# Kernel tuning notes

Measured on AMD Instinct MI355X. Metric: run time of the kernel, lower is better.

## Reference

```python
import jax, jax.numpy as jnp
import numpy as np

HEADS = 16
EPS = 1e-5

def _ln(t):
    # LayerNorm over last axis, no affine params
    mu = jnp.mean(t, axis=-1, keepdims=True)
    var = jnp.var(t, axis=-1, keepdims=True)
    return (t - mu) / jnp.sqrt(var + EPS)

def setup_inputs() -> dict:
    key = jax.random.key(0)
    ks = jax.random.split(key, 8)
    b, n, dim, mlp_dim = 4, 2048, 1024, 4096
    s = lambda d: 1.0 / np.sqrt(d)
    return {
        "x": jax.random.normal(ks[0], (b, n, dim), dtype=jnp.float32),
        "Wqkv": jax.random.uniform(ks[1], (dim, 3 * dim), jnp.float32, -s(dim), s(dim)),
        "W1": jax.random.uniform(ks[2], (dim, mlp_dim), jnp.float32, -s(dim), s(dim)),
        "b1": jax.random.uniform(ks[3], (mlp_dim,), jnp.float32, -s(dim), s(dim)),
        "W2": jax.random.uniform(ks[4], (mlp_dim, dim), jnp.float32, -s(mlp_dim), s(mlp_dim)),
        "b2": jax.random.uniform(ks[5], (dim,), jnp.float32, -s(mlp_dim), s(mlp_dim)),
        "Wout": jax.random.uniform(ks[6], (dim, dim), jnp.float32, -s(dim), s(dim)),
        "bout": jax.random.uniform(ks[7], (dim,), jnp.float32, -s(dim), s(dim)),
    }

def reference(x, Wqkv, W1, b1, W2, b2, Wout, bout):
    b, n, dim = x.shape
    h = HEADS
    d = dim // h
    scale = dim ** (-0.5)  # NOTE: module scales by full dim, not head_dim
    qkv = x @ Wqkv  # [b, n, 3*dim]
    qkv = qkv.reshape(b, n, 3, h, d).transpose(2, 0, 3, 1, 4)  # [3, b, h, n, d]
    q, k, v = qkv[0], qkv[1], qkv[2]
    q, k = _ln(q), _ln(k)
    dots = jnp.einsum('bhid,bhjd->bhij', q, k) * scale
    attn = jax.nn.softmax(dots, axis=-1)
    attn_v = jnp.einsum('bhij,bhjd->bhid', attn, v)
    attn_v = attn_v.transpose(0, 2, 1, 3).reshape(b, n, dim)
    attn_out = attn_v @ Wout + bout
    parallel = jax.nn.gelu(x @ W1 + b1, approximate=False) @ W2 + b2
    return _ln(attn_out + parallel)
```

## Files before the change

### kernel.cpp

```cpp
#include <hip/hip_runtime.h>

typedef __attribute__((ext_vector_type(8))) short s16x8;
typedef __attribute__((ext_vector_type(4))) short s16x4;
typedef __attribute__((ext_vector_type(4))) float f32x4;
typedef __attribute__((ext_vector_type(16))) float f32x16;
typedef __attribute__((ext_vector_type(2))) unsigned uint2v;

#define DEVINL __device__ __forceinline__

DEVINL float b2f(short u){ return __uint_as_float(((unsigned)(unsigned short)u) << 16); }
DEVINL short f2bf(float f){
  unsigned u = __float_as_uint(f);
  u += 0x7fffu + ((u >> 16) & 1u);
  return (short)(u >> 16);
}
DEVINL unsigned cvtpk(float lo, float hi){
  unsigned r;
  asm("v_cvt_pk_bf16_f32 %0, %1, %2" : "=v"(r) : "v"(lo), "v"(hi));
  return r;
}
DEVINL float max3f(float a, float b, float c){
  float r; asm("v_max3_f32 %0, %1, %2, %3" : "=v"(r) : "v"(a), "v"(b), "v"(c)); return r;
}

#if __has_builtin(__builtin_amdgcn_exp2f)
#define EXP2F __builtin_amdgcn_exp2f
#else
#define EXP2F exp2f
#endif

DEVINL f32x4 mfma32(s16x8 a, s16x8 b, f32x4 c){
  return __builtin_amdgcn_mfma_f32_16x16x32_bf16(a, b, c, 0, 0, 0);
}
DEVINL f32x16 mfma3216(s16x8 a, s16x8 b, f32x16 c){
  return __builtin_amdgcn_mfma_f32_32x32x16_bf16(a, b, c, 0, 0, 0);
}

DEVINL uint2v pl32swap(unsigned a, unsigned b){
#if __has_builtin(__builtin_amdgcn_permlane32_swap)
  return __builtin_amdgcn_permlane32_swap(a, b, false, false);
#else
  asm volatile("v_permlane32_swap_b32 %0, %1" : "+v"(a), "+v"(b));
  uint2v r; r[0] = a; r[1] = b; return r;
#endif
}

typedef const unsigned __attribute__((address_space(1)))* gas1;
typedef unsigned __attribute__((address_space(3)))* las3;
DEVINL void gload16(const short* g, short* l){
  __builtin_amdgcn_global_load_lds((gas1)g, (las3)l, 16, 0, 0);
}

#define CFENCE asm volatile("" ::: "memory")
#define PBAR  do{ CFENCE; __builtin_amdgcn_sched_barrier(0); __builtin_amdgcn_s_barrier(); \
                  __builtin_amdgcn_sched_barrier(0); CFENCE; }while(0)
#define VMW8 asm volatile("s_waitcnt vmcnt(8)" ::: "memory")
#define VMW4 asm volatile("s_waitcnt vmcnt(4)" ::: "memory")
#define VMW0 asm volatile("s_waitcnt vmcnt(0)" ::: "memory")
#define PRIO1 __builtin_amdgcn_s_setprio(1)
#define PRIO0 __builtin_amdgcn_s_setprio(0)

static const int Bc   = 4;
static const int Nc   = 2048;
static const int DIM  = 1024;
static const int Tc   = Bc * Nc;
static const int MLP  = 4096;
static const int D3   = 3072;

static const size_t OFF_XB    = 0;
static const size_t OFF_W1T   = 16777216;
static const size_t OFF_QLN   = 25165824;
static const size_t OFF_KLN   = 41943040;
static const size_t OFF_VT    = 58720256;
static const size_t OFF_ATTNV = 75497472;
static const size_t OFF_HB    = 92274688;
static const size_t OFF_WQKVT = OFF_HB;
static const size_t OFF_W2T   = 0;
static const size_t OFF_WOUTT = 8388608;
static const size_t OFF_S2    = OFF_QLN;

DEVINL void transp_body(const float* __restrict__ W, short* __restrict__ Wt,
                        int K, int N, int bid){
  __shared__ float tile[32][33];
  int ntx = N >> 5;
  int tx = bid % ntx, ty = bid / ntx;
  int r = threadIdx.x >> 3, c = (threadIdx.x & 7) * 4;
  f32x4 v = *(const f32x4*)(W + (size_t)(ty*32 + r)*N + tx*32 + c);
  tile[r][c] = v[0]; tile[r][c+1] = v[1]; tile[r][c+2] = v[2]; tile[r][c+3] = v[3];
  __syncthreads();
  s16x4 o;
#pragma unroll
  for (int j = 0; j < 4; ++j) o[j] = f2bf(tile[c+j][r]);
  *(s16x4*)(Wt + (size_t)(tx*32 + r)*K + ty*32 + c) = o;
}

__global__ __launch_bounds__(256) void prep1(const float* __restrict__ x, short* __restrict__ xb,
                                             const float* __restrict__ Wqkv, short* __restrict__ wqkvt,
                                             const float* __restrict__ W1, short* __restrict__ w1t){
  const int b = blockIdx.x;
  if (b < 4096){
    size_t i = ((size_t)b * 256 + threadIdx.x) * 8;
    f32x4 v0 = *(const f32x4*)(x + i);
    f32x4 v1 = *(const f32x4*)(x + i + 4);
    s16x8 o;
#pragma unroll
    for (int j = 0; j < 4; ++j){ o[j] = f2bf(v0[j]); o[4+j] = f2bf(v1[j]); }
    *(s16x8*)(xb + i) = o;
  } else if (b < 7168){
    transp_body(Wqkv, wqkvt, DIM, D3, b - 4096);
  } else {
    transp_body(W1, w1t, DIM, MLP, b - 7168);
  }
}

__global__ __launch_bounds__(256) void prep2(const float* __restrict__ W2, short* __restrict__ w2t,
                                             const float* __restrict__ Wout, short* __restrict__ woutt){
  const int b = blockIdx.x;
  if (b < 4096) transp_body(W2, w2t, MLP, DIM, b);
  else          transp_body(Wout, woutt, DIM, DIM, b - 4096);
}

template<int ACT, int FUSED, int QKVEPI>
__global__ __launch_bounds__(256, 2) void gemmCF(const short* __restrict__ A, const short* __restrict__ A2,
                                                 const short* __restrict__ Bt, const short* __restrict__ Bt2,
                                                 short* __restrict__ C,
                                                 const float* __restrict__ bias, const float* __restrict__ bias2,
                                                 int M, int N, int K1, int K2,
                                                 short* __restrict__ qln, short* __restrict__ kln,
                                                 short* __restrict__ vtb){
  __shared__ short lds[32768];

  const int tid = threadIdx.x;
  const int w = tid >> 6, lane = tid & 63;
  const int lr = lane & 15, g = lane >> 4;
  const int wr = w >> 1, wc = w & 1;
  const int NT1 = K1 >> 6;
  const int NT = NT1 + (FUSED ? (K2 >> 6) : 0);
  const int NIT = NT >> 1;

  const int nbn = N >> 7;
  const int cpx = gridDim.x >> 3;
  const int bid = (int)blockIdx.x;
  const int sw = (bid & 7)*cpx + (bid >> 3);
  const int nbn8 = nbn >> 3;
  const int T8 = sw >> 6, t64 = sw & 63;
  const int bm = (T8 / nbn8)*8 + (t64 >> 3);
  const int bn = (T8 % nbn8)*8 + (t64 & 7);

  const int l2 = lane >> 2;
  const int gsw = ((lane & 3) - ((lane >> 3) & 3)) & 3;
  const int cof = gsw * 8;
  const int qsw8 = ((g + (lr >> 1)) & 3) * 8;

  const short* ap0h = A  + (size_t)(bm*128 + w*16 + l2)*K1 + cof;
  const short* bp0h = Bt + (size_t)(bn*128 + w*16 + l2)*K1 + cof;
  const short* ap0a = FUSED ? (A2  + (size_t)(bm*128 + w*16 + l2)*K2 + cof) : nullptr;
  const short* bp0a = FUSED ? (Bt2 + (size_t)(bn*128 + w*16 + l2)*K2 + cof) : nullptr;

  auto stA = [&](int s, int T_, int kk){
    short* d0 = lds + s*4096 + w*512;
    if (FUSED && T_ >= NT1){
      size_t off = (size_t)(T_ - NT1)*64 + kk*32;
      gload16(ap0a + off, d0);
      gload16(ap0a + (size_t)64*K2 + off, d0 + 2048);
    } else {
      size_t off = (size_t)T_*64 + kk*32;
      gload16(ap0h + off, d0);
      gload16(ap0h + (size_t)64*K1 + off, d0 + 2048);
    }
  };
  auto stB = [&](int s, int T_, int kk){
    short* d0 = lds + 16384 + s*4096 + w*512;
    if (FUSED && T_ >= NT1){
      size_t off = (size_t)(T_ - NT1)*64 + kk*32;
      gload16(bp0a + off, d0);
      gload16(bp0a + (size_t)64*K2 + off, d0 + 2048);
    } else {
      size_t off = (size_t)T_*64 + kk*32;
      gload16(bp0h + off, d0);
      gload16(bp0h + (size_t)64*K1 + off, d0 + 2048);
    }
  };

#define LDA(s, mi) (*(const s16x8*)&lds[(s)*4096 + (wr*64 + (mi)*16 + lr)*32 + qsw8])
#define LDB(s, ni) (*(const s16x8*)&lds[16384 + (s)*4096 + (wc*64 + (ni)*16 + lr)*32 + qsw8])

  f32x4 acc[4][4] = {};
#define MM(ai, r) \
  acc[r][0]=mfma32(ai,b0,acc[r][0]); acc[r][1]=mfma32(ai,b1,acc[r][1]); \
  acc[r][2]=mfma32(ai,b2,acc[r][2]); acc[r][3]=mfma32(ai,b3,acc[r][3]);
#define RD(s) s16x8 a0=LDA(s,0),a1=LDA(s,1),a2=LDA(s,2),a3=LDA(s,3), \
                    b0=LDB(s,0),b1=LDB(s,1),b2=LDB(s,2),b3=LDB(s,3);
#define MM16 MM(a0,0) MM(a1,1) MM(a2,2) MM(a3,3)

  stA(0,0,0); stB(0,0,0);
  stA(1,0,1); stB(1,0,1);
  stA(2,1,0); stB(2,1,0);
  VMW8;
  PBAR;

  for (int i = 0; i < NIT; ++i){
    const int t = i << 1;
    const bool more = (i + 1 < NIT);
    {
      RD(0)
      stA(3, t+1, 1); stB(3, t+1, 1);
      PBAR; PRIO1; MM16 PRIO0;
      VMW8;
      PBAR;
    }
    {
      RD(1)
      if (more){ stA(0, t+2, 0); stB(0, t+2, 0); }
      PBAR; PRIO1; MM16 PRIO0;
      if (more){ VMW8; } else { VMW4; }
      PBAR;
    }
    {
      RD(2)
      if (more){ stA(1, t+2, 1); stB(1, t+2, 1); }
      PBAR; PRIO1; MM16 PRIO0;
      if (more){ VMW8; } else { VMW0; }
      PBAR;
    }
    {
      RD(3)
      if (more){ stA(2, t+3, 0); stB(2, t+3, 0); }
      PBAR; PRIO1; MM16 PRIO0;
      if (more){ VMW8; }
      PBAR;
    }
  }
#undef MM
#undef RD
#undef MM16
#undef LDA
#undef LDB

  if constexpr (QKVEPI){
#pragma unroll
    for (int a = 0; a < 4; ++a){
#pragma unroll
      for (int ni = 0; ni < 4; ++ni){
        const int col = wc*64 + ni*16 + lr;
        f32x4 v = acc[a][ni];
#pragma unroll
        for (int ii = 0; ii < 4; ++ii)
          lds[(wr*64 + a*16 + 4*g + ii)*130 + col] = f2bf(v[ii]);
      }
    }
    __syncthreads();
    const int part = (bn*128) >> 10;
    const int h0 = ((bn*128) & 1023) >> 6;
    const int rg = bm*128;
    const int b = rg >> 11;
    const int tok0 = rg & 2047;

    if (part < 2){
      short* dstbase = part ? kln : qln;
      const float sc = part ? 1.f : 0.04508422003f;
      const int row = tid >> 1, grp = tid & 1;
      const short* src = &lds[row*130 + grp*64];
      float s = 0.f, sq = 0.f;
#pragma unroll
      for (int i2 = 0; i2 < 8; ++i2){
        s16x8 u = *(const s16x8*)(src + i2*8);
#pragma unroll
        for (int j = 0; j < 8; ++j){ float fv = b2f(u[j]); s += fv; sq += fv*fv; }
      }
      const float mu = s * (1.f/64.f);
      const float var = sq * (1.f/64.f) - mu*mu;
      const float inv = rsqrtf(var + 1e-5f) * sc;
      const int bh = b*16 + h0 + grp;
      short* dst = dstbase + ((size_t)bh*Nc + tok0 + row)*64;
#pragma unroll
      for (int i2 = 0; i2 < 8; ++i2){
        s16x8 u = *(const s16x8*)(src + i2*8);
        s16x8 o;
#pragma unroll
        for (int j = 0; j < 8; ++j) o[j] = f2bf((b2f(u[j]) - mu) * inv);
        *(s16x8*)(dst + i2*8) = o;
      }
    } else {
      const int d = tid & 63, hh = (tid >> 6) & 1, half = tid >> 7;
      const int bh = b*16 + h0 + hh;
      short* dst = vtb + ((size_t)bh*64 + d)*Nc + tok0 + half*64;
#pragma unroll
      for (int i2 = 0; i2 < 8; ++i2){
        s16x8 o;
#pragma unroll
        for (int j = 0; j < 8; ++j)
          o[j] = lds[(half*64 + i2*8 + j)*130 + hh*64 + d];
        *(s16x8*)(dst + i2*8) = o;
      }
    }
    return;
  }

#pragma unroll
  for (int a = 0; a < 4; ++a){
#pragma unroll
    for (int ni = 0; ni < 4; ++ni){
      const int col = wc*64 + ni*16 + lr;
      float bv = bias ? bias[bn*128 + col] : 0.f;
      if (FUSED && bias2) bv += bias2[bn*128 + col];
      f32x4 v = acc[a][ni];
#pragma unroll
      for (int ii = 0; ii < 4; ++ii){
        float val = v[ii] + bv;
        if constexpr (ACT) val = 0.5f*val*(1.f + erff(val*0.70710678118f));
        lds[(wr*64 + a*16 + 4*g + ii)*128 + col] = f2bf(val);
      }
    }
  }
  __syncthreads();
  const size_t crow0 = (size_t)bm * 128;
  const int ch = (tid & 15) * 8;
#pragma unroll
  for (int p = 0; p < 8; ++p){
    const int row = p*16 + (tid >> 4);
    *(s16x8*)&C[(crow0 + row)*N + bn*128 + ch] = *(const s16x8*)&lds[row*128 + ch];
  }
}

DEVINL void attn_body(int bid, short* smem,
                      const short* __restrict__ qln, const short* __restrict__ kln,
                      const short* __restrict__ vtb, short* __restrict__ attnv){
  short* Ks = smem;
  short* Vs = smem + 9216;
  const int tid = threadIdx.x;
  const int bh = bid >> 4, qt = bid & 15;
  const int b = bh >> 4, h = bh & 15;
  const int w = tid >> 6, lane = tid & 63;
  const int lq = lane & 31, hi = lane >> 5;
  const int qrow = qt*128 + w*32 + lq;

  const short* qp = qln + ((size_t)bh*Nc + qrow)*64 + hi*8;
  s16x8 qf[4];
#pragma unroll
  for (int m = 0; m < 4; ++m) qf[m] = *(const s16x8*)(qp + m*16);

  f32x16 o0 = {0,0,0,0,0,0,0,0,0,0,0,0,0,0,0,0};
  f32x16 o1 = {0,0,0,0,0,0,0,0,0,0,0,0,0,0,0,0};
  float mrun = -INFINITY, l = 0.f;

  const int sr = tid >> 3;
  const int sc = (tid & 7) * 8;
  const short* kb0 = kln + (size_t)bh*Nc*64;
  const short* vb0 = vtb + (size_t)bh*64*Nc;

  s16x8 kr0, kr1, vr0, vr1;
  {
    kr0 = *(const s16x8*)(kb0 + (size_t)sr*64 + sc);
    kr1 = *(const s16x8*)(kb0 + (size_t)(32 + sr)*64 + sc);
    vr0 = *(const s16x8*)(vb0 + (size_t)sr*Nc + sc);
    vr1 = *(const s16x8*)(vb0 + (size_t)(32 + sr)*Nc + sc);
  }

  for (int kt = 0; kt < 32; ++kt){
    const int cur = kt & 1;
    *(s16x8*)&Ks[cur*4608 + sr*72 + sc]        = kr0;
    *(s16x8*)&Ks[cur*4608 + (32 + sr)*72 + sc] = kr1;
    *(s16x8*)&Vs[cur*4608 + sr*72 + sc]        = vr0;
    *(s16x8*)&Vs[cur*4608 + (32 + sr)*72 + sc] = vr1;
    __syncthreads();
    if (kt + 1 < 32){
      const short* kb = kb0 + (size_t)(kt+1)*64*64;
      const short* vb = vb0 + (kt+1)*64;
      kr0 = *(const s16x8*)(kb + (size_t)sr*64 + sc);
      kr1 = *(const s16x8*)(kb + (size_t)(32 + sr)*64 + sc);
      vr0 = *(const s16x8*)(vb + (size_t)sr*Nc + sc);
      vr1 = *(const s16x8*)(vb + (size_t)(32 + sr)*Nc + sc);
    }

    f32x16 st0 = {0,0,0,0,0,0,0,0,0,0,0,0,0,0,0,0};
    f32x16 st1 = {0,0,0,0,0,0,0,0,0,0,0,0,0,0,0,0};
#pragma unroll
    for (int m = 0; m < 4; ++m){
      s16x8 kf0 = *(const s16x8*)&Ks[cur*4608 +  lq      *72 + m*16 + hi*8];
      s16x8 kf1 = *(const s16x8*)&Ks[cur*4608 + (32 + lq)*72 + m*16 + hi*8];
      st0 = mfma3216(kf0, qf[m], st0);
      st1 = mfma3216(kf1, qf[m], st1);
    }

    float cmax = max3f(st0[0], st0[1], st0[2]);
    cmax = max3f(cmax, st0[3], st0[4]);   cmax = max3f(cmax, st0[5], st0[6]);
    cmax = max3f(cmax, st0[7], st0[8]);   cmax = max3f(cmax, st0[9], st0[10]);
    cmax = max3f(cmax, st0[11], st0[12]); cmax = max3f(cmax, st0[13], st0[14]);
    cmax = max3f(cmax, st0[15], st1[0]);  cmax = max3f(cmax, st1[1], st1[2]);
    cmax = max3f(cmax, st1[3], st1[4]);   cmax = max3f(cmax, st1[5], st1[6]);
    cmax = max3f(cmax, st1[7], st1[8]);   cmax = max3f(cmax, st1[9], st1[10]);
    cmax = max3f(cmax, st1[11], st1[12]); cmax = max3f(cmax, st1[13], st1[14]);
    cmax = fmaxf(cmax, st1[15]);
    cmax = fmaxf(cmax, __shfl_xor(cmax, 32));
    if (__any(cmax > mrun + 8.f)){
      float mnew = fmaxf(mrun, cmax);
      float fr = EXP2F(mrun - mnew);
      l *= fr;
#pragma unroll
      for (int r = 0; r < 16; ++r){ o0[r] *= fr; o1[r] *= fr; }
      mrun = mnew;
    }
    float p0[16], p1[16];
#pragma unroll
    for (int r = 0; r < 16; ++r){
      p0[r] = EXP2F(st0[r] - mrun); l += p0[r];
      p1[r] = EXP2F(st1[r] - mrun); l += p1[r];
    }

#pragma unroll
    for (int kc = 0; kc < 2; ++kc){
      const float* p = kc ? p1 : p0;
#pragma unroll
      for (int kh = 0; kh < 2; ++kh){
        int r0 = kh*8;
        unsigned wa = cvtpk(p[r0+0], p[r0+1]);
        unsigned wb = cvtpk(p[r0+4], p[r0+5]);
        unsigned wc2 = cvtpk(p[r0+2], p[r0+3]);
        unsigned wd = cvtpk(p[r0+6], p[r0+7]);
        uint2v s1 = pl32swap(wa, wb);
        uint2v s2 = pl32swap(wc2, wd);
        union { unsigned u[4]; s16x8 v; } pu;
        pu.u[0] = s1[0]; pu.u[1] = s2[0]; pu.u[2] = s1[1]; pu.u[3] = s2[1];
        s16x8 vf0 = *(const s16x8*)&Vs[cur*4608 +  lq      *72 + kc*32 + kh*16 + hi*8];
        s16x8 vf1 = *(const s16x8*)&Vs[cur*4608 + (32 + lq)*72 + kc*32 + kh*16 + hi*8];
        o0 = mfma3216(vf0, pu.v, o0);
        o1 = mfma3216(vf1, pu.v, o1);
      }
    }
  }

  l += __shfl_xor(l, 32);
  float inv = 1.f / l;
  short* orow = attnv + ((size_t)(b*Nc + qrow))*DIM + h*64;
#pragma unroll
  for (int r = 0; r < 16; r += 2){
    int dv = (r&3) + 8*(r>>2) + 4*hi;
    *(unsigned*)&orow[dv]      = cvtpk(o0[r]*inv, o0[r+1]*inv);
    *(unsigned*)&orow[32 + dv] = cvtpk(o1[r]*inv, o1[r+1]*inv);
  }
}

DEVINL void mlp1_body(int bid, short* lds,
                      const short* __restrict__ A, const short* __restrict__ Bt,
                      short* __restrict__ C, const float* __restrict__ bias){
  const int N = MLP, K1 = DIM;
  const int tid = threadIdx.x;
  const int w = tid >> 6, lane = tid & 63;
  const int lr = lane & 15, g = lane >> 4;
  const int wr = w >> 1, wc = w & 1;
  const int NIT = 8;

  const int nbn = N >> 7;
  const int cpx = 256;
  const int sw = (bid & 7)*cpx + (bid >> 3);
  const int nbn8 = nbn >> 3;
  const int T8 = sw >> 6, t64 = sw & 63;
  const int bm = (T8 / nbn8)*8 + (t64 >> 3);
  const int bn = (T8 % nbn8)*8 + (t64 & 7);

  const int l2 = lane >> 2;
  const int gsw = ((lane & 3) - ((lane >> 3) & 3)) & 3;
  const int cof = gsw * 8;
  const int qsw8 = ((g + (lr >> 1)) & 3) * 8;

  const short* ap0h = A  + (size_t)(bm*128 + w*16 + l2)*K1 + cof;
  const short* bp0h = Bt + (size_t)(bn*128 + w*16 + l2)*K1 + cof;

  auto stA = [&](int s, int T_, int kk){
    short* d0 = lds + s*4096 + w*512;
    size_t off = (size_t)T_*64 + kk*32;
    gload16(ap0h + off, d0);
    gload16(ap0h + (size_t)64*K1 + off, d0 + 2048);
  };
  auto stB = [&](int s, int T_, int kk){
    short* d0 = lds + 16384 + s*4096 + w*512;
    size_t off = (size_t)T_*64 + kk*32;
    gload16(bp0h + off, d0);
    gload16(bp0h + (size_t)64*K1 + off, d0 + 2048);
  };

#define LDA1(s, mi) (*(const s16x8*)&lds[(s)*4096 + (wr*64 + (mi)*16 + lr)*32 + qsw8])
#define LDB1(s, ni) (*(const s16x8*)&lds[16384 + (s)*4096 + (wc*64 + (ni)*16 + lr)*32 + qsw8])

  f32x4 acc[4][4] = {};
#define MM1(ai, r) \
  acc[r][0]=mfma32(ai,b0,acc[r][0]); acc[r][1]=mfma32(ai,b1,acc[r][1]); \
  acc[r][2]=mfma32(ai,b2,acc[r][2]); acc[r][3]=mfma32(ai,b3,acc[r][3]);
#define RD1(s) s16x8 a0=LDA1(s,0),a1=LDA1(s,1),a2=LDA1(s,2),a3=LDA1(s,3), \
                     b0=LDB1(s,0),b1=LDB1(s,1),b2=LDB1(s,2),b3=LDB1(s,3);
#define MM16_1 MM1(a0,0) MM1(a1,1) MM1(a2,2) MM1(a3,3)

  stA(0,0,0); stB(0,0,0);
  stA(1,0,1); stB(1,0,1);
  stA(2,1,0); stB(2,1,0);
  VMW8;
  PBAR;

  for (int i = 0; i < NIT; ++i){
    const int t = i << 1;
    const bool more = (i + 1 < NIT);
    {
      RD1(0)
      stA(3, t+1, 1); stB(3, t+1, 1);
      PBAR; PRIO1; MM16_1 PRIO0;
      VMW8;
      PBAR;
    }
    {
      RD1(1)
      if (more){ stA(0, t+2, 0); stB(0, t+2, 0); }
      PBAR; PRIO1; MM16_1 PRIO0;
      if (more){ VMW8; } else { VMW4; }
      PBAR;
    }
    {
      RD1(2)
      if (more){ stA(1, t+2, 1); stB(1, t+2, 1); }
      PBAR; PRIO1; MM16_1 PRIO0;
      if (more){ VMW8; } else { VMW0; }
      PBAR;
    }
    {
      RD1(3)
      if (more){ stA(2, t+3, 0); stB(2, t+3, 0); }
      PBAR; PRIO1; MM16_1 PRIO0;
      if (more){ VMW8; }
      PBAR;
    }
  }
#undef MM1
#undef RD1
#undef MM16_1
#undef LDA1
#undef LDB1

#pragma unroll
  for (int a = 0; a < 4; ++a){
#pragma unroll
    for (int ni = 0; ni < 4; ++ni){
      const int col = wc*64 + ni*16 + lr;
      const float bv = bias[bn*128 + col];
      f32x4 v = acc[a][ni];
#pragma unroll
      for (int ii = 0; ii < 4; ++ii){
        float val = v[ii] + bv;
        val = 0.5f*val*(1.f + erff(val*0.70710678118f));
        lds[(wr*64 + a*16 + 4*g + ii)*128 + col] = f2bf(val);
      }
    }
  }
  __syncthreads();
  const size_t crow0 = (size_t)bm * 128;
  const int ch = (tid & 15) * 8;
#pragma unroll
  for (int p = 0; p < 8; ++p){
    const int row = p*16 + (tid >> 4);
    *(s16x8*)&C[(crow0 + row)*N + bn*128 + ch] = *(const s16x8*)&lds[row*128 + ch];
  }
}

__global__ __launch_bounds__(256, 2) void attn_mlp1(const short* __restrict__ qln, const short* __restrict__ kln,
                                                    const short* __restrict__ vtb, short* __restrict__ attnv,
                                                    const short* __restrict__ xb, const short* __restrict__ w1t,
                                                    short* __restrict__ hbuf, const float* __restrict__ b1){
  __shared__ short smem[32768];
  const int bid = (int)blockIdx.x;
  if (bid < 1024){
    attn_body(bid, smem, qln, kln, vtb, attnv);
  } else {
    mlp1_body(bid - 1024, smem, xb, w1t, hbuf, b1);
  }
}

__global__ __launch_bounds__(256) void final_ln(const short* __restrict__ s2, float* __restrict__ out){
  __shared__ float red[16];
  int row = blockIdx.x, tid = threadIdx.x;
  size_t base = (size_t)row*DIM + tid*4;
  s16x4 a = *(const s16x4*)(s2 + base);
  float v[4]; float s = 0.f, sq = 0.f;
#pragma unroll
  for (int i = 0; i < 4; ++i){ v[i] = b2f(a[i]); s += v[i]; sq += v[i]*v[i]; }
#pragma unroll
  for (int m = 1; m < 64; m <<= 1){ s += __shfl_xor(s, m); sq += __shfl_xor(sq, m); }
  int wv = tid >> 6;
  if ((tid & 63) == 0){ red[wv] = s; red[8 + wv] = sq; }
  __syncthreads();
  if (tid == 0){
    float S = red[0] + red[1] + red[2] + red[3];
    float Q = red[8] + red[9] + red[10] + red[11];
    float mu = S * (1.f/1024.f);
    float var = Q * (1.f/1024.f) - mu*mu;
    red[12] = mu; red[13] = rsqrtf(var + 1e-5f);
  }
  __syncthreads();
  float mu = red[12], inv = red[13];
#pragma unroll
  for (int i = 0; i < 4; ++i) out[base + i] = (v[i] - mu) * inv;
}

extern "C" void kernel_launch(void* const* d_in, const int* in_sizes, int n_in,
                              void* d_out, int out_size, void* d_ws, size_t ws_size,
                              hipStream_t stream){
  const float* x    = (const float*)d_in[0];
  const float* Wqkv = (const float*)d_in[1];
  const float* W1   = (const float*)d_in[2];
  const float* b1   = (const float*)d_in[3];
  const float* W2   = (const float*)d_in[4];
  const float* b2   = (const float*)d_in[5];
  const float* Wout = (const float*)d_in[6];
  const float* bout = (const float*)d_in[7];
  float* out = (float*)d_out;
  char* ws = (char*)d_ws;

  short* xb    = (short*)(ws + OFF_XB);
  short* w1t   = (short*)(ws + OFF_W1T);
  short* wqkvt = (short*)(ws + OFF_WQKVT);
  short* qln   = (short*)(ws + OFF_QLN);
  short* kln   = (short*)(ws + OFF_KLN);
  short* vtb   = (short*)(ws + OFF_VT);
  short* attnv = (short*)(ws + OFF_ATTNV);
  short* hbuf  = (short*)(ws + OFF_HB);
  short* w2t   = (short*)(ws + OFF_W2T);
  short* woutt = (short*)(ws + OFF_WOUTT);
  short* s2    = (short*)(ws + OFF_S2);

  prep1<<<11264, 256, 0, stream>>>(x, xb, Wqkv, wqkvt, W1, w1t);

  gemmCF<0,0,1><<<(Tc/128)*(D3/128), 256, 0, stream>>>(xb, xb, wqkvt, wqkvt, nullptr,
                                                       nullptr, nullptr, Tc, D3, DIM, DIM,
                                                       qln, kln, vtb);

  attn_mlp1<<<1024 + 2048, 256, 0, stream>>>(qln, kln, vtb, attnv, xb, w1t, hbuf, b1);

  prep2<<<5120, 256, 0, stream>>>(W2, w2t, Wout, woutt);

  gemmCF<0,1,0><<<(Tc/128)*(DIM/128), 256, 0, stream>>>(hbuf, attnv, w2t, woutt, s2,
                                                        b2, bout, Tc, DIM, MLP, DIM,
                                                        nullptr, nullptr, nullptr);

  final_ln<<<Tc, 256, 0, stream>>>(s2, out);
}
```

Before: 377.0 us.

## Overlap W1 transpose with QKV GEMM in a combined kernel launch

Moves the W1 fp32-to-bf16 transpose out of the first prep kernel and into the same launch as the QKV projection GEMM, with extra blocks after the GEMM tiles handling the transpose through shared memory. The QKV GEMM becomes a specialized device body with compile-time constants, and the tile-swizzle constants in the MLP1 body are hardcoded. The aim is to hide the bandwidth-bound transpose behind the compute-bound GEMM and shorten the serial prep stage. In exchange the combined kernel shares LDS and occupancy limits between the two kinds of block, and the transpose blocks run after the GEMM tiles in dispatch order.

New measurement: 377.7 us, median of 2. No clear change (+0.2%).

```diff
diff --git a/kernel.cpp b/kernel.cpp
--- a/kernel.cpp
+++ b/kernel.cpp
@@ -94,9 +94,22 @@
   *(s16x4*)(Wt + (size_t)(tx*32 + r)*K + ty*32 + c) = o;
 }
 
+DEVINL void transp_body_p(const float* __restrict__ W, short* __restrict__ Wt,
+                          int K, int N, int bid, float* tile){
+  int ntx = N >> 5;
+  int tx = bid % ntx, ty = bid / ntx;
+  int r = threadIdx.x >> 3, c = (threadIdx.x & 7) * 4;
+  f32x4 v = *(const f32x4*)(W + (size_t)(ty*32 + r)*N + tx*32 + c);
+  tile[r*33 + c] = v[0]; tile[r*33 + c+1] = v[1]; tile[r*33 + c+2] = v[2]; tile[r*33 + c+3] = v[3];
+  __syncthreads();
+  s16x4 o;
+#pragma unroll
+  for (int j = 0; j < 4; ++j) o[j] = f2bf(tile[(c+j)*33 + r]);
+  *(s16x4*)(Wt + (size_t)(tx*32 + r)*K + ty*32 + c) = o;
+}
+
 __global__ __launch_bounds__(256) void prep1(const float* __restrict__ x, short* __restrict__ xb,
-                                             const float* __restrict__ Wqkv, short* __restrict__ wqkvt,
-                                             const float* __restrict__ W1, short* __restrict__ w1t){
+                                             const float* __restrict__ Wqkv, short* __restrict__ wqkvt){
   const int b = blockIdx.x;
   if (b < 4096){
     size_t i = ((size_t)b * 256 + threadIdx.x) * 8;
@@ -106,10 +119,8 @@
 #pragma unroll
     for (int j = 0; j < 4; ++j){ o[j] = f2bf(v0[j]); o[4+j] = f2bf(v1[j]); }
     *(s16x8*)(xb + i) = o;
-  } else if (b < 7168){
+  } else {
     transp_body(Wqkv, wqkvt, DIM, D3, b - 4096);
-  } else {
-    transp_body(W1, w1t, DIM, MLP, b - 7168);
   }
 }
 
@@ -120,14 +131,177 @@
   else          transp_body(Wout, woutt, DIM, DIM, b - 4096);
 }
 
-template<int ACT, int FUSED, int QKVEPI>
+DEVINL void qkv_body(int bid, short* lds,
+                     const short* __restrict__ A, const short* __restrict__ Bt,
+                     short* __restrict__ qln, short* __restrict__ kln,
+                     short* __restrict__ vtb){
+  const int N = D3, K1 = DIM;
+  const int tid = threadIdx.x;
+  const int w = tid >> 6, lane = tid & 63;
+  const int lr = lane & 15, g = lane >> 4;
+  const int wr = w >> 1, wc = w & 1;
+  const int NIT = 8;
+
+  const int cpx = 192;
+  const int sw = (bid & 7)*cpx + (bid >> 3);
+  const int nbn8 = 3;
+  const int T8 = sw >> 6, t64 = sw & 63;
+  const int bm = (T8 / nbn8)*8 + (t64 >> 3);
+  const int bn = (T8 % nbn8)*8 + (t64 & 7);
+
+  const int l2 = lane >> 2;
+  const int gsw = ((lane & 3) - ((lane >> 3) & 3)) & 3;
+  const int cof = gsw * 8;
+  const int qsw8 = ((g + (lr >> 1)) & 3) * 8;
+
+  const short* ap0h = A  + (size_t)(bm*128 + w*16 + l2)*K1 + cof;
+  const short* bp0h = Bt + (size_t)(bn*128 + w*16 + l2)*K1 + cof;
+
+  auto stA = [&](int s, int T_, int kk){
+    short* d0 = lds + s*4096 + w*512;
+    size_t off = (size_t)T_*64 + kk*32;
+    gload16(ap0h + off, d0);
+    gload16(ap0h + (size_t)64*K1 + off, d0 + 2048);
+  };
+  auto stB = [&](int s, int T_, int kk){
+    short* d0 = lds + 16384 + s*4096 + w*512;
+    size_t off = (size_t)T_*64 + kk*32;
+    gload16(bp0h + off, d0);
+    gload16(bp0h + (size_t)64*K1 + off, d0 + 2048);
+  };
+
+#define LDAQ(s, mi) (*(const s16x8*)&lds[(s)*4096 + (wr*64 + (mi)*16 + lr)*32 + qsw8])
+#define LDBQ(s, ni) (*(const s16x8*)&lds[16384 + (s)*4096 + (wc*64 + (ni)*16 + lr)*32 + qsw8])
+
+  f32x4 acc[4][4] = {};
+#define MMQ(ai, r) \
+  acc[r][0]=mfma32(ai,b0,acc[r][0]); acc[r][1]=mfma32(ai,b1,acc[r][1]); \
+  acc[r][2]=mfma32(ai,b2,acc[r][2]); acc[r][3]=mfma32(ai,b3,acc[r][3]);
+#define RDQ(s) s16x8 a0=LDAQ(s,0),a1=LDAQ(s,1),a2=LDAQ(s,2),a3=LDAQ(s,3), \
+                     b0=LDBQ(s,0),b1=LDBQ(s,1),b2=LDBQ(s,2),b3=LDBQ(s,3);
+#define MM16Q MMQ(a0,0) MMQ(a1,1) MMQ(a2,2) MMQ(a3,3)
+
+  stA(0,0,0); stB(0,0,0);
+  stA(1,0,1); stB(1,0,1);
+  stA(2,1,0); stB(2,1,0);
+  VMW8;
+  PBAR;
+
+  for (int i = 0; i < NIT; ++i){
+    const int t = i << 1;
+    const bool more = (i + 1 < NIT);
+    {
+      RDQ(0)
+      stA(3, t+1, 1); stB(3, t+1, 1);
+      PBAR; PRIO1; MM16Q PRIO0;
+      VMW8;
+      PBAR;
+    }
+    {
+      RDQ(1)
+      if (more){ stA(0, t+2, 0); stB(0, t+2, 0); }
+      PBAR; PRIO1; MM16Q PRIO0;
+      if (more){ VMW8; } else { VMW4; }
+      PBAR;
+    }
+    {
+      RDQ(2)
+      if (more){ stA(1, t+2, 1); stB(1, t+2, 1); }
+      PBAR; PRIO1; MM16Q PRIO0;
+      if (more){ VMW8; } else { VMW0; }
+      PBAR;
+    }
+    {
+      RDQ(3)
+      if (more){ stA(2, t+3, 0); stB(2, t+3, 0); }
+      PBAR; PRIO1; MM16Q PRIO0;
+      if (more){ VMW8; }
+      PBAR;
+    }
+  }
+#undef MMQ
+#undef RDQ
+#undef MM16Q
+#undef LDAQ
+#undef LDBQ
+
+#pragma unroll
+  for (int a = 0; a < 4; ++a){
+#pragma unroll
+    for (int ni = 0; ni < 4; ++ni){
+      const int col = wc*64 + ni*16 + lr;
+      f32x4 v = acc[a][ni];
+#pragma unroll
+      for (int ii = 0; ii < 4; ++ii)
+        lds[(wr*64 + a*16 + 4*g + ii)*130 + col] = f2bf(v[ii]);
+    }
+  }
+  __syncthreads();
+  const int part = (bn*128) >> 10;
+  const int h0 = ((bn*128) & 1023) >> 6;
+  const int rg = bm*128;
+  const int b = rg >> 11;
+  const int tok0 = rg & 2047;
+
+  if (part < 2){
+    short* dstbase = part ? kln : qln;
+    const float sc = part ? 1.f : 0.04508422003f;
+    const int row = tid >> 1, grp = tid & 1;
+    const short* src = &lds[row*130 + grp*64];
+    float s = 0.f, sq = 0.f;
+#pragma unroll
+    for (int i2 = 0; i2 < 8; ++i2){
+      s16x8 u = *(const s16x8*)(src + i2*8);
+#pragma unroll
+      for (int j = 0; j < 8; ++j){ float fv = b2f(u[j]); s += fv; sq += fv*fv; }
+    }
+    const float mu = s * (1.f/64.f);
+    const float var = sq * (1.f/64.f) - mu*mu;
+    const float inv = rsqrtf(var + 1e-5f) * sc;
+    const int bh = b*16 + h0 + grp;
+    short* dst = dstbase + ((size_t)bh*Nc + tok0 + row)*64;
+#pragma unroll
+    for (int i2 = 0; i2 < 8; ++i2){
+      s16x8 u = *(const s16x8*)(src + i2*8);
+      s16x8 o;
+#pragma unroll
+      for (int j = 0; j < 8; ++j) o[j] = f2bf((b2f(u[j]) - mu) * inv);
+      *(s16x8*)(dst + i2*8) = o;
+    }
+  } else {
+    const int d = tid & 63, hh = (tid >> 6) & 1, half = tid >> 7;
+    const int bh = b*16 + h0 + hh;
+    short* dst = vtb + ((size_t)bh*64 + d)*Nc + tok0 + half*64;
+#pragma unroll
+    for (int i2 = 0; i2 < 8; ++i2){
+      s16x8 o;
+#pragma unroll
+      for (int j = 0; j < 8; ++j)
+        o[j] = lds[(half*64 + i2*8 + j)*130 + hh*64 + d];
+      *(s16x8*)(dst + i2*8) = o;
+    }
+  }
+}
+
+__global__ __launch_bounds__(256, 2) void qkv_w1t(const short* __restrict__ xb, const short* __restrict__ wqkvt,
+                                                  short* __restrict__ qln, short* __restrict__ kln,
+                                                  short* __restrict__ vtb,
+                                                  const float* __restrict__ W1, short* __restrict__ w1t){
+  __shared__ short smem[32768];
+  const int bid = (int)blockIdx.x;
+  if (bid < 1536){
+    qkv_body(bid, smem, xb, wqkvt, qln, kln, vtb);
+  } else {
+    transp_body_p(W1, w1t, DIM, MLP, bid - 1536, (float*)smem);
+  }
+}
+
+template<int ACT, int FUSED>
 __global__ __launch_bounds__(256, 2) void gemmCF(const short* __restrict__ A, const short* __restrict__ A2,
                                                  const short* __restrict__ Bt, const short* __restrict__ Bt2,
                                                  short* __restrict__ C,
                                                  const float* __restrict__ bias, const float* __restrict__ bias2,
-                                                 int M, int N, int K1, int K2,
-                                                 short* __restrict__ qln, short* __restrict__ kln,
-                                                 short* __restrict__ vtb){
+                                                 int M, int N, int K1, int K2){
   __shared__ short lds[32768];
 
   const int tid = threadIdx.x;
@@ -236,66 +410,6 @@
 #undef MM16
 #undef LDA
 #undef LDB
-
-  if constexpr (QKVEPI){
-#pragma unroll
-    for (int a = 0; a < 4; ++a){
-#pragma unroll
-      for (int ni = 0; ni < 4; ++ni){
-        const int col = wc*64 + ni*16 + lr;
-        f32x4 v = acc[a][ni];
-#pragma unroll
-        for (int ii = 0; ii < 4; ++ii)
-          lds[(wr*64 + a*16 + 4*g + ii)*130 + col] = f2bf(v[ii]);
-      }
-    }
-    __syncthreads();
-    const int part = (bn*128) >> 10;
-    const int h0 = ((bn*128) & 1023) >> 6;
-    const int rg = bm*128;
-    const int b = rg >> 11;
-    const int tok0 = rg & 2047;
-
-    if (part < 2){
-      short* dstbase = part ? kln : qln;
-      const float sc = part ? 1.f : 0.04508422003f;
-      const int row = tid >> 1, grp = tid & 1;
-      const short* src = &lds[row*130 + grp*64];
-      float s = 0.f, sq = 0.f;
-#pragma unroll
-      for (int i2 = 0; i2 < 8; ++i2){
-        s16x8 u = *(const s16x8*)(src + i2*8);
-#pragma unroll
-        for (int j = 0; j < 8; ++j){ float fv = b2f(u[j]); s += fv; sq += fv*fv; }
-      }
-      const float mu = s * (1.f/64.f);
-      const float var = sq * (1.f/64.f) - mu*mu;
-      const float inv = rsqrtf(var + 1e-5f) * sc;
-      const int bh = b*16 + h0 + grp;
-      short* dst = dstbase + ((size_t)bh*Nc + tok0 + row)*64;
-#pragma unroll
-      for (int i2 = 0; i2 < 8; ++i2){
-        s16x8 u = *(const s16x8*)(src + i2*8);
-        s16x8 o;
-#pragma unroll
-        for (int j = 0; j < 8; ++j) o[j] = f2bf((b2f(u[j]) - mu) * inv);
-        *(s16x8*)(dst + i2*8) = o;
-      }
-    } else {
-      const int d = tid & 63, hh = (tid >> 6) & 1, half = tid >> 7;
-      const int bh = b*16 + h0 + hh;
-      short* dst = vtb + ((size_t)bh*64 + d)*Nc + tok0 + half*64;
-#pragma unroll
-      for (int i2 = 0; i2 < 8; ++i2){
-        s16x8 o;
-#pragma unroll
-        for (int j = 0; j < 8; ++j)
-          o[j] = lds[(half*64 + i2*8 + j)*130 + hh*64 + d];
-        *(s16x8*)(dst + i2*8) = o;
-      }
-    }
-    return;
-  }
 
 #pragma unroll
   for (int a = 0; a < 4; ++a){
@@ -451,10 +565,9 @@
   const int wr = w >> 1, wc = w & 1;
   const int NIT = 8;
 
-  const int nbn = N >> 7;
   const int cpx = 256;
   const int sw = (bid & 7)*cpx + (bid >> 3);
-  const int nbn8 = nbn >> 3;
+  const int nbn8 = 4;
   const int T8 = sw >> 6, t64 = sw & 63;
   const int bm = (T8 / nbn8)*8 + (t64 >> 3);
   const int bn = (T8 % nbn8)*8 + (t64 & 7);
@@ -625,19 +738,16 @@
   short* woutt = (short*)(ws + OFF_WOUTT);
   short* s2    = (short*)(ws + OFF_S2);
 
-  prep1<<<11264, 256, 0, stream>>>(x, xb, Wqkv, wqkvt, W1, w1t);
-
-  gemmCF<0,0,1><<<(Tc/128)*(D3/128), 256, 0, stream>>>(xb, xb, wqkvt, wqkvt, nullptr,
-                                                       nullptr, nullptr, Tc, D3, DIM, DIM,
-                                                       qln, kln, vtb);
+  prep1<<<7168, 256, 0, stream>>>(x, xb, Wqkv, wqkvt);
+
+  qkv_w1t<<<1536 + 4096, 256, 0, stream>>>(xb, wqkvt, qln, kln, vtb, W1, w1t);
 
   attn_mlp1<<<1024 + 2048, 256, 0, stream>>>(qln, kln, vtb, attnv, xb, w1t, hbuf, b1);
 
   prep2<<<5120, 256, 0, stream>>>(W2, w2t, Wout, woutt);
 
-  gemmCF<0,1,0><<<(Tc/128)*(DIM/128), 256, 0, stream>>>(hbuf, attnv, w2t, woutt, s2,
-                                                        b2, bout, Tc, DIM, MLP, DIM,
-                                                        nullptr, nullptr, nullptr);
+  gemmCF<0,1><<<(Tc/128)*(DIM/128), 256, 0, stream>>>(hbuf, attnv, w2t, woutt, s2,
+                                                      b2, bout, Tc, DIM, MLP, DIM);
 
   final_ln<<<Tc, 256, 0, stream>>>(s2, out);
 }
```
